# Kernel optimization log

Hardware: AMD Instinct MI355X
Metric: run time of the kernel (lower is better)

## Reference

```python
import jax, jax.numpy as jnp
import numpy as np

N_ENT = 100000
N_REL = 200
D_IN = 128
D_HID = 128
D_OUT = 128
N_BASES = 50
N_EDGES = 800000
N_TRIPLES = 4096
BN_EPS = 1e-5


def setup_inputs() -> dict:
    key = jax.random.key(0)
    ks = jax.random.split(key, 16)
    xavier = lambda k, shape: jax.random.normal(k, shape, jnp.float32) * np.sqrt(2.0 / (shape[-2] + shape[-1]))
    inp = {
        'entity_embeds': xavier(ks[0], (N_ENT, D_IN)),
        'bases': xavier(ks[1], (N_BASES, D_IN)),
        'coefficients': xavier(ks[2], (N_REL, N_BASES)),
        'self_rel_embed': xavier(ks[3], (1, D_IN)),
        'W1': xavier(ks[4], (3, D_IN, D_HID)),
        'relw1': xavier(ks[5], (D_IN, D_HID)),
        'bn1_gamma': jnp.ones((D_HID,), jnp.float32),
        'bn1_beta': jnp.zeros((D_HID,), jnp.float32),
        'W2': xavier(ks[6], (3, D_HID, D_OUT)),
        'relw2': xavier(ks[7], (D_HID, D_OUT)),
        'bn2_gamma': jnp.ones((D_OUT,), jnp.float32),
        'bn2_beta': jnp.zeros((D_OUT,), jnp.float32),
        'ent_ids': jnp.arange(N_ENT, dtype=jnp.int32),
        'edge_index': jax.random.randint(ks[8], (2, N_EDGES), 0, N_ENT, jnp.int32),
        'edge_type': jax.random.randint(ks[9], (N_EDGES,), 0, 2 * N_REL + 1, jnp.int32),
        'y': jax.random.randint(ks[10], (N_EDGES,), 0, 3, jnp.int32),
    }
    heads = jax.random.randint(ks[11], (N_TRIPLES,), 0, N_ENT, jnp.int32)
    rels = jax.random.randint(ks[12], (N_TRIPLES,), 0, 2 * N_REL + 1, jnp.int32)
    tails = jax.random.randint(ks[13], (N_TRIPLES,), 0, N_ENT, jnp.int32)
    inp['triples'] = jnp.stack([heads, rels, tails], axis=1)
    return inp


def _compgcn_layer(x, r, edge_index, edge_type, y, W, relw, gamma, beta):
    src, dst = edge_index[0], edge_index[1]
    # message: gather neighbor & relation embeds, edge-direction-conditioned matmul
    msgs = x[src] - r[edge_type]                      # [E, d_in]
    out = jnp.zeros((msgs.shape[0], W.shape[-1]), msgs.dtype)
    for k in range(3):  # y in {0,1,2}: masked matmul instead of [E,d,d] gather
        mask = (y == k)[:, None]
        out = out + jnp.where(mask, msgs, 0.0) @ W[k]
    # scatter-add aggregation at destination nodes
    agg = jax.ops.segment_sum(out, dst, num_segments=x.shape[0])  # [N, d_out]
    # BatchNorm1d (training-mode batch statistics, biased var)
    mean = jnp.mean(agg, axis=0)
    var = jnp.mean(jnp.square(agg - mean), axis=0)
    bn = (agg - mean) * jax.lax.rsqrt(var + BN_EPS) * gamma + beta
    return jnp.tanh(bn), r @ relw


def reference(entity_embeds, bases, coefficients, self_rel_embed, W1, relw1,
              bn1_gamma, bn1_beta, W2, relw2, bn2_gamma, bn2_beta,
              ent_ids, edge_index, edge_type, y, triples):
    x = entity_embeds[ent_ids]
    r = coefficients @ bases                           # basis-composed relations
    r = jnp.concatenate([r, -r, self_rel_embed], axis=0)  # [2R+1, d]
    x, r = _compgcn_layer(x, r, edge_index, edge_type, y, W1, relw1, bn1_gamma, bn1_beta)
    x, r = _compgcn_layer(x, r, edge_index, edge_type, y, W2, relw2, bn2_gamma, bn2_beta)
    # decode: TransE-style L1 score
    h = x[triples[:, 0]]
    re = r[triples[:, 1]]
    t = x[triples[:, 2]]
    scores = jnp.sum(jnp.abs(h + re - t), axis=1)      # p=1 norm
    return scores
```

## Files before the change

### kernel.cpp

```cpp
#include <hip/hip_runtime.h>
#include <cstdint>

typedef __attribute__((ext_vector_type(8))) short short8;
typedef __attribute__((ext_vector_type(4))) float f32x4;

static __device__ __forceinline__ unsigned short f2bf(float f) {
  unsigned int u = __float_as_uint(f);
  unsigned int r = (u + 0x7FFFu + ((u >> 16) & 1u)) >> 16;
  return (unsigned short)r;
}
static __device__ __forceinline__ unsigned int pack2bf(float a, float b) {
  return (unsigned int)f2bf(a) | ((unsigned int)f2bf(b) << 16);
}
static __device__ __forceinline__ float2 bf2f(unsigned int u) {
  return make_float2(__uint_as_float(u << 16), __uint_as_float(u & 0xFFFF0000u));
}
static __device__ __forceinline__ void acc8(float* a, uint4 h, uint4 r) {
  float2 f, g;
  f = bf2f(h.x); g = bf2f(r.x); a[0] += f.x - g.x; a[1] += f.y - g.y;
  f = bf2f(h.y); g = bf2f(r.y); a[2] += f.x - g.x; a[3] += f.y - g.y;
  f = bf2f(h.z); g = bf2f(r.z); a[4] += f.x - g.x; a[5] += f.y - g.y;
  f = bf2f(h.w); g = bf2f(r.w); a[6] += f.x - g.x; a[7] += f.y - g.y;
}

__global__ __launch_bounds__(256) void k_prep(
    const float* __restrict__ coeff, const float* __restrict__ bases,
    const float* __restrict__ selfr, const float* __restrict__ relw1,
    const float* __restrict__ relw2,
    unsigned int* __restrict__ rfb, unsigned int* __restrict__ r1b,
    float* __restrict__ r2,
    const float* __restrict__ W1, const float* __restrict__ W2,
    unsigned short* __restrict__ WT1, unsigned short* __restrict__ WT2,
    const float* __restrict__ ent, const int* __restrict__ ent_ids,
    unsigned int* __restrict__ entbf,
    int* __restrict__ counts, float* __restrict__ stats,
    int nPairs, int nKeys, int cvtB, int cntB) {
  int b = blockIdx.x, tid = threadIdx.x;
  if (b < 201) {
    __shared__ float row[2][128], r1row[2][128];
    int half = tid >> 7, c = tid & 127;
    int r = 2 * b + half;
    bool ok = (r <= 400);
    if (ok) {
      float v;
      if (r == 400) {
        v = selfr[c];
      } else {
        int rr = (r < 200) ? r : r - 200;
        float s = 0.f;
#pragma unroll 10
        for (int k = 0; k < 50; ++k) s += coeff[rr * 50 + k] * bases[k * 128 + c];
        v = (r < 200) ? s : -s;
      }
      row[half][c] = v;
    }
    __syncthreads();
    if (ok && c < 64) rfb[r * 64 + c] = pack2bf(row[half][2 * c], row[half][2 * c + 1]);
    if (ok) {
      float s = 0.f;
#pragma unroll 8
      for (int k = 0; k < 128; ++k) s += row[half][k] * relw1[k * 128 + c];
      r1row[half][c] = s;
    }
    __syncthreads();
    if (ok && c < 64) r1b[r * 64 + c] = pack2bf(r1row[half][2 * c], r1row[half][2 * c + 1]);
    if (ok) {
      float s = 0.f;
#pragma unroll 8
      for (int k = 0; k < 128; ++k) s += r1row[half][k] * relw2[k * 128 + c];
      r2[r * 128 + c] = s;
    }
  } else if (b < 585) {
    int idx = (b - 201) * 256 + tid;
    const int half = 128 * 384;
    const float* W = (idx < half) ? W1 : W2;
    unsigned short* WT = (idx < half) ? WT1 : WT2;
    int id2 = (idx < half) ? idx : idx - half;
    int n = id2 & 127, k = id2 >> 7;
    int kk = k >> 7, kr = k & 127;
    WT[(size_t)n * 384 + k] = f2bf(W[(size_t)kk * 16384 + kr * 128 + n]);
  } else if (b < 585 + cvtB) {
    int i = (b - 585) * 256 + tid;
    if (i < nPairs) {
      int e = i >> 6;
      int src = ent_ids[e];
      float2 v = *(const float2*)&ent[(size_t)src * 128 + (i & 63) * 2];
      entbf[i] = pack2bf(v.x, v.y);
    }
  } else if (b < 585 + cvtB + cntB) {
    int i = (b - (585 + cvtB)) * 256 + tid;
    if (i < nKeys) counts[i] = 0;
  } else {
    int i = (b - (585 + cvtB + cntB)) * 256 + tid;
    if (i < 16896) stats[i] = 0.f;
  }
}

__global__ __launch_bounds__(256) void k_histR(const int* __restrict__ ei, const int* __restrict__ y,
                                               int* __restrict__ counts, int nE, int rsz) {
  int r = blockIdx.x;
  int e0 = blockIdx.y * 1024;
#pragma unroll
  for (int i = 0; i < 4; ++i) {
    int e = e0 + i * 256 + threadIdx.x;
    if (e < nE) {
      int key = ei[nE + e] * 3 + y[e];
      if (key / rsz == r) atomicAdd(&counts[key], 1);
    }
  }
}

__global__ void k_scan1(const int* __restrict__ counts, int* __restrict__ local,
                        int* __restrict__ blockSums, int n) {
  __shared__ int sdata[1024];
  int tid = threadIdx.x;
  int i = blockIdx.x * 1024 + tid;
  int v = (i < n) ? counts[i] : 0;
  sdata[tid] = v;
  __syncthreads();
  for (int off = 1; off < 1024; off <<= 1) {
    int t = (tid >= off) ? sdata[tid - off] : 0;
    __syncthreads();
    sdata[tid] += t;
    __syncthreads();
  }
  if (i < n) local[i] = sdata[tid] - v;
  if (tid == 1023) blockSums[blockIdx.x] = sdata[1023];
}

__global__ void k_scan2(const int* __restrict__ blockSums, int* __restrict__ carries,
                        int* __restrict__ offsets, int n, int nb) {
  __shared__ int sdata[1024];
  int tid = threadIdx.x;
  int v = (tid < nb) ? blockSums[tid] : 0;
  sdata[tid] = v;
  __syncthreads();
  for (int off = 1; off < 1024; off <<= 1) {
    int t = (tid >= off) ? sdata[tid - off] : 0;
    __syncthreads();
    sdata[tid] += t;
    __syncthreads();
  }
  if (tid < nb) carries[tid] = sdata[tid] - v;
  if (tid == 1023) offsets[n] = sdata[1023];
}

__global__ void k_scan3(const int* __restrict__ local, const int* __restrict__ carries,
                        int* __restrict__ offsets, int* __restrict__ cursor, int n) {
  int i = blockIdx.x * 1024 + threadIdx.x;
  if (i >= n) return;
  int v = local[i] + carries[blockIdx.x];
  offsets[i] = v;
  cursor[i] = v;
}

__global__ __launch_bounds__(256) void k_fillR(const int* __restrict__ ei, const int* __restrict__ et,
                                               const int* __restrict__ y, int* __restrict__ cursor,
                                               unsigned int* __restrict__ bucket, int nE, int rsz) {
  int r = blockIdx.x;
  int e0 = blockIdx.y * 1024;
#pragma unroll
  for (int i = 0; i < 4; ++i) {
    int e = e0 + i * 256 + threadIdx.x;
    if (e < nE) {
      int key = ei[nE + e] * 3 + y[e];
      if (key / rsz == r) {
        int slot = atomicAdd(&cursor[key], 1);
        bucket[slot] = (unsigned int)ei[e] | ((unsigned int)et[e] << 20);
      }
    }
  }
}

__global__ __launch_bounds__(256, 6) void k_fused(
    const unsigned int* __restrict__ xb, const unsigned int* __restrict__ rb,
    const int* __restrict__ offsets, const unsigned int* __restrict__ packed,
    const unsigned short* __restrict__ WT, unsigned short* __restrict__ C,
    float* __restrict__ statsRep, int M) {
  __shared__ unsigned short As[32][392];
  __shared__ float sSum[128], sSq[128];
  const int tid = threadIdx.x;
  const int m0 = blockIdx.x * 32;
  const int wave = tid >> 6, lane = tid & 63;
  const int quad = lane >> 4, l16 = lane & 15;
  const int qid = (wave << 2) | quad;
  if (tid < 128) { sSum[tid] = 0.f; sSq[tid] = 0.f; }

#pragma unroll 1
  for (int i = 0; i < 6; ++i) {
    int kloc = qid * 6 + i;
    int dloc = kloc / 3, cls = kloc - dloc * 3;
    float a0[8] = {}, a1[8] = {};
    int dst = m0 + dloc;
    if (dst < M) {
      int key = dst * 3 + cls;
      int s = offsets[key], e = offsets[key + 1];
      int j = s;
      for (; j + 1 < e; j += 2) {
        unsigned int p0 = packed[j], p1 = packed[j + 1];
        int s0 = p0 & 0xFFFFF, t0 = p0 >> 20;
        int s1 = p1 & 0xFFFFF, t1 = p1 >> 20;
        uint4 h0 = *(const uint4*)&xb[(size_t)s0 * 64 + l16 * 4];
        uint4 r0 = *(const uint4*)&rb[(size_t)t0 * 64 + l16 * 4];
        uint4 h1 = *(const uint4*)&xb[(size_t)s1 * 64 + l16 * 4];
        uint4 r1 = *(const uint4*)&rb[(size_t)t1 * 64 + l16 * 4];
        acc8(a0, h0, r0);
        acc8(a1, h1, r1);
      }
      if (j < e) {
        unsigned int p0 = packed[j];
        int s0 = p0 & 0xFFFFF, t0 = p0 >> 20;
        uint4 h0 = *(const uint4*)&xb[(size_t)s0 * 64 + l16 * 4];
        uint4 r0 = *(const uint4*)&rb[(size_t)t0 * 64 + l16 * 4];
        acc8(a0, h0, r0);
      }
    }
    uint4 o;
    o.x = pack2bf(a0[0] + a1[0], a0[1] + a1[1]);
    o.y = pack2bf(a0[2] + a1[2], a0[3] + a1[3]);
    o.z = pack2bf(a0[4] + a1[4], a0[5] + a1[5]);
    o.w = pack2bf(a0[6] + a1[6], a0[7] + a1[7]);
    *(uint4*)&As[dloc][cls * 128 + l16 * 8] = o;
  }
  __syncthreads();

  const unsigned short* Wp = WT + (size_t)(wave * 32 + l16) * 384 + quad * 8;
  short8 bc0 = *(const short8*)(Wp);
  short8 bc1 = *(const short8*)(Wp + 16 * 384);
  f32x4 acc[2][2] = {};
#pragma unroll 1
  for (int it = 0; it < 12; ++it) {
    short8 bn0, bn1;
    if (it < 11) {
      bn0 = *(const short8*)(Wp + (it + 1) * 32);
      bn1 = *(const short8*)(Wp + 16 * 384 + (it + 1) * 32);
    }
    short8 a[2];
#pragma unroll
    for (int t = 0; t < 2; ++t) a[t] = *(const short8*)&As[t * 16 + l16][it * 32 + quad * 8];
#pragma unroll
    for (int t = 0; t < 2; ++t) {
      acc[t][0] = __builtin_amdgcn_mfma_f32_16x16x32_bf16(a[t], bc0, acc[t][0], 0, 0, 0);
      acc[t][1] = __builtin_amdgcn_mfma_f32_16x16x32_bf16(a[t], bc1, acc[t][1], 0, 0, 0);
    }
    if (it < 11) { bc0 = bn0; bc1 = bn1; }
  }

  float ps[2] = {}, pq[2] = {};
#pragma unroll
  for (int t = 0; t < 2; ++t) {
#pragma unroll
    for (int reg = 0; reg < 4; ++reg) {
      int m = m0 + t * 16 + quad * 4 + reg;
      if (m < M) {
#pragma unroll
        for (int ct = 0; ct < 2; ++ct) {
          float v = acc[t][ct][reg];
          int col = wave * 32 + ct * 16 + l16;
          C[(size_t)m * 128 + col] = f2bf(v);
          ps[ct] += v; pq[ct] += v * v;
        }
      }
    }
  }
#pragma unroll
  for (int ct = 0; ct < 2; ++ct) {
    int col = wave * 32 + ct * 16 + l16;
    atomicAdd(&sSum[col], ps[ct]);
    atomicAdd(&sSq[col], pq[ct]);
  }
  __syncthreads();
  if (tid < 128) {
    float* rep = statsRep + ((blockIdx.x & 31) << 8);
    atomicAdd(&rep[tid], sSum[tid]);
    atomicAdd(&rep[128 + tid], sSq[tid]);
  }
}

__global__ void k_collapse(const float* __restrict__ rep, float* __restrict__ fin) {
  int c = threadIdx.x;
  float s = 0.f;
#pragma unroll
  for (int r = 0; r < 32; ++r) s += rep[r * 256 + c];
  fin[c] = s;
}

__global__ void k_norm(const uint4* __restrict__ Cb4,
                       const float* __restrict__ sums, const float* __restrict__ sumsq,
                       const float* __restrict__ gamma, const float* __restrict__ beta,
                       float invN, uint4* __restrict__ xb4, int nQuad) {
  __shared__ float sc_s[128], bi_s[128];
  if (threadIdx.x < 128) {
    int c = threadIdx.x;
    float mean = sums[c] * invN;
    float var = fmaxf(sumsq[c] * invN - mean * mean, 0.f);
    float sc = rsqrtf(var + 1e-5f) * gamma[c];
    sc_s[c] = sc;
    bi_s[c] = beta[c] - mean * sc;
  }
  __syncthreads();
  int i = blockIdx.x * blockDim.x + threadIdx.x;
  if (i >= nQuad) return;
  uint4 v = Cb4[i];
  int j = (i * 4) & 63;
  uint4 o;
  float2 f;
  f = bf2f(v.x);
  o.x = pack2bf(tanhf(fmaf(f.x, sc_s[2*j],   bi_s[2*j])),   tanhf(fmaf(f.y, sc_s[2*j+1], bi_s[2*j+1])));
  f = bf2f(v.y);
  o.y = pack2bf(tanhf(fmaf(f.x, sc_s[2*j+2], bi_s[2*j+2])), tanhf(fmaf(f.y, sc_s[2*j+3], bi_s[2*j+3])));
  f = bf2f(v.z);
  o.z = pack2bf(tanhf(fmaf(f.x, sc_s[2*j+4], bi_s[2*j+4])), tanhf(fmaf(f.y, sc_s[2*j+5], bi_s[2*j+5])));
  f = bf2f(v.w);
  o.w = pack2bf(tanhf(fmaf(f.x, sc_s[2*j+6], bi_s[2*j+6])), tanhf(fmaf(f.y, sc_s[2*j+7], bi_s[2*j+7])));
  xb4[i] = o;
}

__global__ void k_score(const unsigned int* __restrict__ xb, const float* __restrict__ r,
                        const int* __restrict__ triples, float* __restrict__ out, int nT) {
  int gid = blockIdx.x * blockDim.x + threadIdx.x;
  int t = gid >> 6;
  if (t >= nT) return;
  int lane = gid & 63;
  int h = triples[t * 3], rel = triples[t * 3 + 1], tl = triples[t * 3 + 2];
  float2 a = bf2f(xb[(size_t)h * 64 + lane]);
  float2 b = *(const float2*)&r[(size_t)rel * 128 + lane * 2];
  float2 cc = bf2f(xb[(size_t)tl * 64 + lane]);
  float s = fabsf(a.x + b.x - cc.x) + fabsf(a.y + b.y - cc.y);
#pragma unroll
  for (int off = 32; off > 0; off >>= 1) s += __shfl_down(s, off);
  if (lane == 0) out[t] = s;
}

extern "C" void kernel_launch(void* const* d_in, const int* in_sizes, int n_in,
                              void* d_out, int out_size, void* d_ws, size_t ws_size,
                              hipStream_t stream) {
  const float* ent   = (const float*)d_in[0];
  const float* bases = (const float*)d_in[1];
  const float* coeff = (const float*)d_in[2];
  const float* selfr = (const float*)d_in[3];
  const float* W1    = (const float*)d_in[4];
  const float* relw1 = (const float*)d_in[5];
  const float* g1    = (const float*)d_in[6];
  const float* b1    = (const float*)d_in[7];
  const float* W2    = (const float*)d_in[8];
  const float* relw2 = (const float*)d_in[9];
  const float* g2    = (const float*)d_in[10];
  const float* b2    = (const float*)d_in[11];
  const int* ent_ids = (const int*)d_in[12];
  const int* ei      = (const int*)d_in[13];
  const int* et      = (const int*)d_in[14];
  const int* yk      = (const int*)d_in[15];
  const int* triples = (const int*)d_in[16];

  const int M  = in_sizes[0] / 128;
  const int nE = in_sizes[14];
  const int nT = in_sizes[16] / 3;
  const int nKeys = M * 3;
  const int nScanBlocks = (nKeys + 1023) / 1024;
  const int rsz = (nKeys + 7) / 8;

  float* p = (float*)d_ws;
  float* r2    = p; p += 401 * 128;
  float* statsAll = p; p += 16896;
  float* rep1 = statsAll;
  float* rep2 = statsAll + 32 * 256;
  float* fin1 = statsAll + 64 * 256;
  float* fin2 = fin1 + 256;
  unsigned short* Cb  = (unsigned short*)p;
  unsigned int* entbf = (unsigned int*)(Cb + (size_t)M * 128);
  unsigned int* xb    = entbf + (size_t)M * 64;
  unsigned int* rfb   = xb + (size_t)M * 64;
  unsigned int* r1b   = rfb + 401 * 64;
  unsigned short* WT1 = (unsigned short*)(r1b + 401 * 64);
  unsigned short* WT2 = WT1 + 128 * 384;
  int* counts  = (int*)(WT2 + 128 * 384);
  int* offsets = counts + nKeys;
  int* cursor  = offsets + nKeys + 1;
  int* slocal  = cursor + nKeys;
  int* sblock  = slocal + nKeys;
  int* scarry  = sblock + nScanBlocks;
  unsigned int* bucket = (unsigned int*)(scarry + nScanBlocks);

  float* out = (float*)d_out;

  const int nPairs = M * 64;
  const int nQuad  = M * 16;
  const int cvtB = (nPairs + 255) / 256;
  const int cntB = (nKeys + 255) / 256;
  const int zeroB = 66;
  const int prepBlocks = 585 + cvtB + cntB + zeroB;
  const int fusedBlocks = (M + 31) / 32;
  const int normBlocks = (nQuad + 255) / 256;
  const dim3 rangedGrid(8, (nE + 1023) / 1024);

  k_prep<<<prepBlocks, 256, 0, stream>>>(coeff, bases, selfr, relw1, relw2,
                                         rfb, r1b, r2, W1, W2, WT1, WT2,
                                         ent, ent_ids, entbf, counts, statsAll,
                                         nPairs, nKeys, cvtB, cntB);

  k_histR<<<rangedGrid, 256, 0, stream>>>(ei, yk, counts, nE, rsz);
  k_scan1<<<nScanBlocks, 1024, 0, stream>>>(counts, slocal, sblock, nKeys);
  k_scan2<<<1, 1024, 0, stream>>>(sblock, scarry, offsets, nKeys, nScanBlocks);
  k_scan3<<<nScanBlocks, 1024, 0, stream>>>(slocal, scarry, offsets, cursor, nKeys);
  k_fillR<<<rangedGrid, 256, 0, stream>>>(ei, et, yk, cursor, bucket, nE, rsz);

  k_fused<<<fusedBlocks, 256, 0, stream>>>(entbf, rfb, offsets, bucket, WT1,
                                           Cb, rep1, M);
  k_collapse<<<1, 256, 0, stream>>>(rep1, fin1);
  k_norm<<<normBlocks, 256, 0, stream>>>((const uint4*)Cb, fin1, fin1 + 128, g1, b1,
                                         1.0f / M, (uint4*)xb, nQuad);

  k_fused<<<fusedBlocks, 256, 0, stream>>>(xb, r1b, offsets, bucket, WT2,
                                           Cb, rep2, M);
  k_collapse<<<1, 256, 0, stream>>>(rep2, fin2);
  k_norm<<<normBlocks, 256, 0, stream>>>((const uint4*)Cb, fin2, fin2 + 128, g2, b2,
                                         1.0f / M, (uint4*)xb, nQuad);

  k_score<<<(nT * 64 + 255) / 256, 256, 0, stream>>>(xb, r2, triples, out, nT);
}
```

Baseline: 432.6 us.

## Process edge classes sequentially with a smaller shared tile to raise occupancy

The fused gather+MFMA kernel now loops over the three edge classes. For each class it gathers 32 rows by 128 columns into a shared tile, then runs the four k-steps of the matmul against that class's slice of W. This shrinks shared memory from 32x392 to 32x136 bf16, and launch bounds go from 6 to 8 blocks per CU. The aim is more resident waves to hide gather latency, paid for with two extra barriers per class and less independent gather work per thread between syncs.

After: 450.1 us. 4.1% more time.

```diff
diff --git a/kernel.cpp b/kernel.cpp
--- a/kernel.cpp
+++ b/kernel.cpp
@@ -172,12 +172,12 @@
   }
 }
 
-__global__ __launch_bounds__(256, 6) void k_fused(
+__global__ __launch_bounds__(256, 8) void k_fused(
     const unsigned int* __restrict__ xb, const unsigned int* __restrict__ rb,
     const int* __restrict__ offsets, const unsigned int* __restrict__ packed,
     const unsigned short* __restrict__ WT, unsigned short* __restrict__ C,
     float* __restrict__ statsRep, int M) {
-  __shared__ unsigned short As[32][392];
+  __shared__ unsigned short As[32][136];
   __shared__ float sSum[128], sSq[128];
   const int tid = threadIdx.x;
   const int m0 = blockIdx.x * 32;
@@ -186,64 +186,61 @@
   const int qid = (wave << 2) | quad;
   if (tid < 128) { sSum[tid] = 0.f; sSq[tid] = 0.f; }
 
+  f32x4 acc[2][2] = {};
+  const unsigned short* Wp = WT + (size_t)(wave * 32 + l16) * 384 + quad * 8;
+
 #pragma unroll 1
-  for (int i = 0; i < 6; ++i) {
-    int kloc = qid * 6 + i;
-    int dloc = kloc / 3, cls = kloc - dloc * 3;
-    float a0[8] = {}, a1[8] = {};
-    int dst = m0 + dloc;
-    if (dst < M) {
-      int key = dst * 3 + cls;
-      int s = offsets[key], e = offsets[key + 1];
-      int j = s;
-      for (; j + 1 < e; j += 2) {
-        unsigned int p0 = packed[j], p1 = packed[j + 1];
-        int s0 = p0 & 0xFFFFF, t0 = p0 >> 20;
-        int s1 = p1 & 0xFFFFF, t1 = p1 >> 20;
-        uint4 h0 = *(const uint4*)&xb[(size_t)s0 * 64 + l16 * 4];
-        uint4 r0 = *(const uint4*)&rb[(size_t)t0 * 64 + l16 * 4];
-        uint4 h1 = *(const uint4*)&xb[(size_t)s1 * 64 + l16 * 4];
-        uint4 r1 = *(const uint4*)&rb[(size_t)t1 * 64 + l16 * 4];
-        acc8(a0, h0, r0);
-        acc8(a1, h1, r1);
+  for (int cls = 0; cls < 3; ++cls) {
+#pragma unroll 1
+    for (int i = 0; i < 2; ++i) {
+      int dloc = 2 * qid + i;
+      float a0[8] = {}, a1[8] = {};
+      int dst = m0 + dloc;
+      if (dst < M) {
+        int key = dst * 3 + cls;
+        int s = offsets[key], e = offsets[key + 1];
+        int j = s;
+        for (; j + 1 < e; j += 2) {
+          unsigned int p0 = packed[j], p1 = packed[j + 1];
+          int s0 = p0 & 0xFFFFF, t0 = p0 >> 20;
+          int s1 = p1 & 0xFFFFF, t1 = p1 >> 20;
+          uint4 h0 = *(const uint4*)&xb[(size_t)s0 * 64 + l16 * 4];
+          uint4 r0 = *(const uint4*)&rb[(size_t)t0 * 64 + l16 * 4];
+          uint4 h1 = *(const uint4*)&xb[(size_t)s1 * 64 + l16 * 4];
+          uint4 r1 = *(const uint4*)&rb[(size_t)t1 * 64 + l16 * 4];
+          acc8(a0, h0, r0);
+          acc8(a1, h1, r1);
+        }
+        if (j < e) {
+          unsigned int p0 = packed[j];
+          int s0 = p0 & 0xFFFFF, t0 = p0 >> 20;
+          uint4 h0 = *(const uint4*)&xb[(size_t)s0 * 64 + l16 * 4];
+          uint4 r0 = *(const uint4*)&rb[(size_t)t0 * 64 + l16 * 4];
+          acc8(a0, h0, r0);
+        }
       }
-      if (j < e) {
-        unsigned int p0 = packed[j];
-        int s0 = p0 & 0xFFFFF, t0 = p0 >> 20;
-        uint4 h0 = *(const uint4*)&xb[(size_t)s0 * 64 + l16 * 4];
-        uint4 r0 = *(const uint4*)&rb[(size_t)t0 * 64 + l16 * 4];
-        acc8(a0, h0, r0);
-      }
-    }
-    uint4 o;
-    o.x = pack2bf(a0[0] + a1[0], a0[1] + a1[1]);
-    o.y = pack2bf(a0[2] + a1[2], a0[3] + a1[3]);
-    o.z = pack2bf(a0[4] + a1[4], a0[5] + a1[5]);
-    o.w = pack2bf(a0[6] + a1[6], a0[7] + a1[7]);
-    *(uint4*)&As[dloc][cls * 128 + l16 * 8] = o;
-  }
-  __syncthreads();
-
-  const unsigned short* Wp = WT + (size_t)(wave * 32 + l16) * 384 + quad * 8;
-  short8 bc0 = *(const short8*)(Wp);
-  short8 bc1 = *(const short8*)(Wp + 16 * 384);
-  f32x4 acc[2][2] = {};
-#pragma unroll 1
-  for (int it = 0; it < 12; ++it) {
-    short8 bn0, bn1;
-    if (it < 11) {
-      bn0 = *(const short8*)(Wp + (it + 1) * 32);
-      bn1 = *(const short8*)(Wp + 16 * 384 + (it + 1) * 32);
-    }
-    short8 a[2];
-#pragma unroll
-    for (int t = 0; t < 2; ++t) a[t] = *(const short8*)&As[t * 16 + l16][it * 32 + quad * 8];
-#pragma unroll
-    for (int t = 0; t < 2; ++t) {
-      acc[t][0] = __builtin_amdgcn_mfma_f32_16x16x32_bf16(a[t], bc0, acc[t][0], 0, 0, 0);
-      acc[t][1] = __builtin_amdgcn_mfma_f32_16x16x32_bf16(a[t], bc1, acc[t][1], 0, 0, 0);
-    }
-    if (it < 11) { bc0 = bn0; bc1 = bn1; }
+      uint4 o;
+      o.x = pack2bf(a0[0] + a1[0], a0[1] + a1[1]);
+      o.y = pack2bf(a0[2] + a1[2], a0[3] + a1[3]);
+      o.z = pack2bf(a0[4] + a1[4], a0[5] + a1[5]);
+      o.w = pack2bf(a0[6] + a1[6], a0[7] + a1[7]);
+      *(uint4*)&As[dloc][l16 * 8] = o;
+    }
+    __syncthreads();
+
+    const unsigned short* Wc = Wp + cls * 128;
+#pragma unroll
+    for (int k = 0; k < 4; ++k) {
+      short8 b0 = *(const short8*)(Wc + k * 32);
+      short8 b1 = *(const short8*)(Wc + 16 * 384 + k * 32);
+      short8 a0 = *(const short8*)&As[l16][k * 32 + quad * 8];
+      short8 a1 = *(const short8*)&As[16 + l16][k * 32 + quad * 8];
+      acc[0][0] = __builtin_amdgcn_mfma_f32_16x16x32_bf16(a0, b0, acc[0][0], 0, 0, 0);
+      acc[0][1] = __builtin_amdgcn_mfma_f32_16x16x32_bf16(a0, b1, acc[0][1], 0, 0, 0);
+      acc[1][0] = __builtin_amdgcn_mfma_f32_16x16x32_bf16(a1, b0, acc[1][0], 0, 0, 0);
+      acc[1][1] = __builtin_amdgcn_mfma_f32_16x16x32_bf16(a1, b1, acc[1][1], 0, 0, 0);
+    }
+    __syncthreads();
   }
 
   float ps[2] = {}, pq[2] = {};
```

## Fuse both layers, BN and scoring into one cooperative persistent kernel

Applied to the files above, without the earlier changes.

Replaces the per-layer fused/collapse/norm/score launch sequence with a single cooperative kernel of 1024 blocks, each owning up to four 32-row tiles. The MFMA accumulators stay in registers across a grid-wide sync, so BatchNorm plus tanh are applied directly from registers. This removes the intermediate C buffer round trip and several kernel launches. In exchange it adds grid.sync barriers, higher register pressure from 64 accumulator vectors per thread, and lower occupancy. It keeps a fallback to the old path if the cooperative launch fails.

After: 994.4 us. +129.9%, slower.

```diff
diff --git a/kernel.cpp b/kernel.cpp
--- a/kernel.cpp
+++ b/kernel.cpp
@@ -1,5 +1,8 @@
 #include <hip/hip_runtime.h>
+#include <hip/hip_cooperative_groups.h>
 #include <cstdint>
+
+namespace cg = cooperative_groups;
 
 typedef __attribute__((ext_vector_type(8))) short short8;
 typedef __attribute__((ext_vector_type(4))) float f32x4;
@@ -172,6 +175,200 @@
   }
 }
 
+static __device__ __forceinline__ void gather96(
+    const unsigned int* __restrict__ xb, const unsigned int* __restrict__ rb,
+    const int* __restrict__ offsets, const unsigned int* __restrict__ packed,
+    unsigned short (*As)[392], int m0, int qid, int l16) {
+#pragma unroll 1
+  for (int i = 0; i < 6; ++i) {
+    int kloc = qid * 6 + i;
+    int dloc = kloc / 3, cls = kloc - dloc * 3;
+    float a0[8] = {}, a1[8] = {};
+    int key = (m0 + dloc) * 3 + cls;
+    int s = offsets[key], e = offsets[key + 1];
+    int j = s;
+    for (; j + 1 < e; j += 2) {
+      unsigned int p0 = packed[j], p1 = packed[j + 1];
+      int s0 = p0 & 0xFFFFF, t0 = p0 >> 20;
+      int s1 = p1 & 0xFFFFF, t1 = p1 >> 20;
+      uint4 h0 = *(const uint4*)&xb[(size_t)s0 * 64 + l16 * 4];
+      uint4 r0 = *(const uint4*)&rb[(size_t)t0 * 64 + l16 * 4];
+      uint4 h1 = *(const uint4*)&xb[(size_t)s1 * 64 + l16 * 4];
+      uint4 r1 = *(const uint4*)&rb[(size_t)t1 * 64 + l16 * 4];
+      acc8(a0, h0, r0);
+      acc8(a1, h1, r1);
+    }
+    if (j < e) {
+      unsigned int p0 = packed[j];
+      int s0 = p0 & 0xFFFFF, t0 = p0 >> 20;
+      uint4 h0 = *(const uint4*)&xb[(size_t)s0 * 64 + l16 * 4];
+      uint4 r0 = *(const uint4*)&rb[(size_t)t0 * 64 + l16 * 4];
+      acc8(a0, h0, r0);
+    }
+    uint4 o;
+    o.x = pack2bf(a0[0] + a1[0], a0[1] + a1[1]);
+    o.y = pack2bf(a0[2] + a1[2], a0[3] + a1[3]);
+    o.z = pack2bf(a0[4] + a1[4], a0[5] + a1[5]);
+    o.w = pack2bf(a0[6] + a1[6], a0[7] + a1[7]);
+    *(uint4*)&As[dloc][cls * 128 + l16 * 8] = o;
+  }
+}
+
+struct MegaArgs {
+  const unsigned int* entbf;
+  const unsigned int* rfb;
+  const unsigned int* r1b;
+  const int* offsets;
+  const unsigned int* packed;
+  const unsigned short* WT1;
+  const unsigned short* WT2;
+  float* rep1;
+  float* rep2;
+  const float* g1; const float* b1;
+  const float* g2; const float* b2;
+  unsigned short* xb1;
+  unsigned short* xb2;
+  const float* r2;
+  const int* triples;
+  float* out;
+  int nTiles; int nT; float invN;
+};
+
+static __device__ __forceinline__ void layer_pass(
+    const MegaArgs& A,
+    const unsigned int* __restrict__ xbin, const unsigned int* __restrict__ rbin,
+    const unsigned short* __restrict__ WT, float* __restrict__ rep,
+    const float* __restrict__ gamma, const float* __restrict__ beta,
+    unsigned short* __restrict__ xbout,
+    unsigned short (*As)[392], float* sSum, float* sSq,
+    float* sc_s, float* bi_s, cg::grid_group& grid) {
+  const int tid = threadIdx.x;
+  const int wave = tid >> 6, lane = tid & 63;
+  const int quad = lane >> 4, l16 = lane & 15;
+  const int qid = (wave << 2) | quad;
+  const f32x4 vz = {0.f, 0.f, 0.f, 0.f};
+  f32x4 acc[4][2][2];
+#pragma unroll
+  for (int t = 0; t < 4; ++t)
+#pragma unroll
+    for (int a = 0; a < 2; ++a)
+#pragma unroll
+      for (int b = 0; b < 2; ++b) acc[t][a][b] = vz;
+
+  if (tid < 128) { sSum[tid] = 0.f; sSq[tid] = 0.f; }
+  __syncthreads();
+
+  const unsigned short* Wp = WT + (size_t)(wave * 32 + l16) * 384 + quad * 8;
+
+#pragma unroll
+  for (int t = 0; t < 4; ++t) {
+    int tile = blockIdx.x + t * 1024;
+    bool valid = tile < A.nTiles;
+    if (valid) gather96(xbin, rbin, A.offsets, A.packed, As, tile * 32, qid, l16);
+    __syncthreads();
+    if (valid) {
+      short8 bc0 = *(const short8*)(Wp);
+      short8 bc1 = *(const short8*)(Wp + 16 * 384);
+#pragma unroll 1
+      for (int it = 0; it < 12; ++it) {
+        short8 bn0, bn1;
+        if (it < 11) {
+          bn0 = *(const short8*)(Wp + (it + 1) * 32);
+          bn1 = *(const short8*)(Wp + 16 * 384 + (it + 1) * 32);
+        }
+        short8 a0 = *(const short8*)&As[l16][it * 32 + quad * 8];
+        short8 a1 = *(const short8*)&As[16 + l16][it * 32 + quad * 8];
+        acc[t][0][0] = __builtin_amdgcn_mfma_f32_16x16x32_bf16(a0, bc0, acc[t][0][0], 0, 0, 0);
+        acc[t][0][1] = __builtin_amdgcn_mfma_f32_16x16x32_bf16(a0, bc1, acc[t][0][1], 0, 0, 0);
+        acc[t][1][0] = __builtin_amdgcn_mfma_f32_16x16x32_bf16(a1, bc0, acc[t][1][0], 0, 0, 0);
+        acc[t][1][1] = __builtin_amdgcn_mfma_f32_16x16x32_bf16(a1, bc1, acc[t][1][1], 0, 0, 0);
+        if (it < 11) { bc0 = bn0; bc1 = bn1; }
+      }
+      float ps[2] = {}, pq[2] = {};
+#pragma unroll
+      for (int tr = 0; tr < 2; ++tr)
+#pragma unroll
+        for (int reg = 0; reg < 4; ++reg)
+#pragma unroll
+          for (int ct = 0; ct < 2; ++ct) {
+            float v = acc[t][tr][ct][reg];
+            ps[ct] += v; pq[ct] += v * v;
+          }
+#pragma unroll
+      for (int ct = 0; ct < 2; ++ct) {
+        int col = wave * 32 + ct * 16 + l16;
+        atomicAdd(&sSum[col], ps[ct]);
+        atomicAdd(&sSq[col], pq[ct]);
+      }
+    }
+    __syncthreads();
+  }
+  if (tid < 128) {
+    float* rp = rep + ((blockIdx.x & 31) << 8);
+    atomicAdd(&rp[tid], sSum[tid]);
+    atomicAdd(&rp[128 + tid], sSq[tid]);
+  }
+  grid.sync();
+
+  if (tid < 128) {
+    float s = 0.f, q = 0.f;
+#pragma unroll
+    for (int r = 0; r < 32; ++r) { s += rep[r * 256 + tid]; q += rep[r * 256 + 128 + tid]; }
+    float mean = s * A.invN;
+    float var = fmaxf(q * A.invN - mean * mean, 0.f);
+    float sc = rsqrtf(var + 1e-5f) * gamma[tid];
+    sc_s[tid] = sc;
+    bi_s[tid] = beta[tid] - mean * sc;
+  }
+  __syncthreads();
+
+#pragma unroll
+  for (int t = 0; t < 4; ++t) {
+    int tile = blockIdx.x + t * 1024;
+    if (tile < A.nTiles) {
+      int m0 = tile * 32;
+#pragma unroll
+      for (int tr = 0; tr < 2; ++tr)
+#pragma unroll
+        for (int reg = 0; reg < 4; ++reg) {
+          int m = m0 + tr * 16 + quad * 4 + reg;
+#pragma unroll
+          for (int ct = 0; ct < 2; ++ct) {
+            int col = wave * 32 + ct * 16 + l16;
+            float f = tanhf(fmaf(acc[t][tr][ct][reg], sc_s[col], bi_s[col]));
+            xbout[(size_t)m * 128 + col] = f2bf(f);
+          }
+        }
+    }
+  }
+  grid.sync();
+}
+
+__global__ __launch_bounds__(256, 4) void k_mega(MegaArgs A) {
+  __shared__ unsigned short As[32][392];
+  __shared__ float sSum[128], sSq[128], sc_s[128], bi_s[128];
+  cg::grid_group grid = cg::this_grid();
+
+  layer_pass(A, A.entbf, A.rfb, A.WT1, A.rep1, A.g1, A.b1, A.xb1,
+             As, sSum, sSq, sc_s, bi_s, grid);
+  layer_pass(A, (const unsigned int*)A.xb1, A.r1b, A.WT2, A.rep2, A.g2, A.b2, A.xb2,
+             As, sSum, sSq, sc_s, bi_s, grid);
+
+  int gw = blockIdx.x * 4 + (threadIdx.x >> 6);
+  if (gw < A.nT) {
+    int lane = threadIdx.x & 63;
+    const unsigned int* xbu = (const unsigned int*)A.xb2;
+    int h = A.triples[gw * 3], rel = A.triples[gw * 3 + 1], tl = A.triples[gw * 3 + 2];
+    float2 a = bf2f(xbu[(size_t)h * 64 + lane]);
+    float2 b = *(const float2*)&A.r2[(size_t)rel * 128 + lane * 2];
+    float2 c = bf2f(xbu[(size_t)tl * 64 + lane]);
+    float s = fabsf(a.x + b.x - c.x) + fabsf(a.y + b.y - c.y);
+#pragma unroll
+    for (int off = 32; off > 0; off >>= 1) s += __shfl_down(s, off);
+    if (lane == 0) A.out[gw] = s;
+  }
+}
+
 __global__ __launch_bounds__(256, 6) void k_fused(
     const unsigned int* __restrict__ xb, const unsigned int* __restrict__ rb,
     const int* __restrict__ offsets, const unsigned int* __restrict__ packed,
@@ -185,45 +382,8 @@
   const int quad = lane >> 4, l16 = lane & 15;
   const int qid = (wave << 2) | quad;
   if (tid < 128) { sSum[tid] = 0.f; sSq[tid] = 0.f; }
-
-#pragma unroll 1
-  for (int i = 0; i < 6; ++i) {
-    int kloc = qid * 6 + i;
-    int dloc = kloc / 3, cls = kloc - dloc * 3;
-    float a0[8] = {}, a1[8] = {};
-    int dst = m0 + dloc;
-    if (dst < M) {
-      int key = dst * 3 + cls;
-      int s = offsets[key], e = offsets[key + 1];
-      int j = s;
-      for (; j + 1 < e; j += 2) {
-        unsigned int p0 = packed[j], p1 = packed[j + 1];
-        int s0 = p0 & 0xFFFFF, t0 = p0 >> 20;
-        int s1 = p1 & 0xFFFFF, t1 = p1 >> 20;
-        uint4 h0 = *(const uint4*)&xb[(size_t)s0 * 64 + l16 * 4];
-        uint4 r0 = *(const uint4*)&rb[(size_t)t0 * 64 + l16 * 4];
-        uint4 h1 = *(const uint4*)&xb[(size_t)s1 * 64 + l16 * 4];
-        uint4 r1 = *(const uint4*)&rb[(size_t)t1 * 64 + l16 * 4];
-        acc8(a0, h0, r0);
-        acc8(a1, h1, r1);
-      }
-      if (j < e) {
-        unsigned int p0 = packed[j];
-        int s0 = p0 & 0xFFFFF, t0 = p0 >> 20;
-        uint4 h0 = *(const uint4*)&xb[(size_t)s0 * 64 + l16 * 4];
-        uint4 r0 = *(const uint4*)&rb[(size_t)t0 * 64 + l16 * 4];
-        acc8(a0, h0, r0);
-      }
-    }
-    uint4 o;
-    o.x = pack2bf(a0[0] + a1[0], a0[1] + a1[1]);
-    o.y = pack2bf(a0[2] + a1[2], a0[3] + a1[3]);
-    o.z = pack2bf(a0[4] + a1[4], a0[5] + a1[5]);
-    o.w = pack2bf(a0[6] + a1[6], a0[7] + a1[7]);
-    *(uint4*)&As[dloc][cls * 128 + l16 * 8] = o;
-  }
-  __syncthreads();
-
+  gather96(xb, rb, offsets, packed, As, m0, qid, l16);
+  __syncthreads();
   const unsigned short* Wp = WT + (size_t)(wave * 32 + l16) * 384 + quad * 8;
   short8 bc0 = *(const short8*)(Wp);
   short8 bc1 = *(const short8*)(Wp + 16 * 384);
@@ -235,20 +395,17 @@
       bn0 = *(const short8*)(Wp + (it + 1) * 32);
       bn1 = *(const short8*)(Wp + 16 * 384 + (it + 1) * 32);
     }
-    short8 a[2];
-#pragma unroll
-    for (int t = 0; t < 2; ++t) a[t] = *(const short8*)&As[t * 16 + l16][it * 32 + quad * 8];
-#pragma unroll
-    for (int t = 0; t < 2; ++t) {
-      acc[t][0] = __builtin_amdgcn_mfma_f32_16x16x32_bf16(a[t], bc0, acc[t][0], 0, 0, 0);
-      acc[t][1] = __builtin_amdgcn_mfma_f32_16x16x32_bf16(a[t], bc1, acc[t][1], 0, 0, 0);
-    }
+    short8 a0 = *(const short8*)&As[l16][it * 32 + quad * 8];
+    short8 a1 = *(const short8*)&As[16 + l16][it * 32 + quad * 8];
+    acc[0][0] = __builtin_amdgcn_mfma_f32_16x16x32_bf16(a0, bc0, acc[0][0], 0, 0, 0);
+    acc[0][1] = __builtin_amdgcn_mfma_f32_16x16x32_bf16(a0, bc1, acc[0][1], 0, 0, 0);
+    acc[1][0] = __builtin_amdgcn_mfma_f32_16x16x32_bf16(a1, bc0, acc[1][0], 0, 0, 0);
+    acc[1][1] = __builtin_amdgcn_mfma_f32_16x16x32_bf16(a1, bc1, acc[1][1], 0, 0, 0);
     if (it < 11) { bc0 = bn0; bc1 = bn1; }
   }
-
   float ps[2] = {}, pq[2] = {};
 #pragma unroll
-  for (int t = 0; t < 2; ++t) {
+  for (int t = 0; t < 2; ++t)
 #pragma unroll
     for (int reg = 0; reg < 4; ++reg) {
       int m = m0 + t * 16 + quad * 4 + reg;
@@ -262,7 +419,6 @@
         }
       }
     }
-  }
 #pragma unroll
   for (int ct = 0; ct < 2; ++ct) {
     int col = wave * 32 + ct * 16 + l16;
@@ -368,9 +524,10 @@
   float* fin1 = statsAll + 64 * 256;
   float* fin2 = fin1 + 256;
   unsigned short* Cb  = (unsigned short*)p;
-  unsigned int* entbf = (unsigned int*)(Cb + (size_t)M * 128);
-  unsigned int* xb    = entbf + (size_t)M * 64;
-  unsigned int* rfb   = xb + (size_t)M * 64;
+  unsigned short* xb1 = Cb + (size_t)M * 128;
+  unsigned short* xb2 = xb1 + (size_t)M * 128;
+  unsigned int* entbf = (unsigned int*)(xb2 + (size_t)M * 128);
+  unsigned int* rfb   = entbf + (size_t)M * 64;
   unsigned int* r1b   = rfb + 401 * 64;
   unsigned short* WT1 = (unsigned short*)(r1b + 401 * 64);
   unsigned short* WT2 = WT1 + 128 * 384;
@@ -390,8 +547,7 @@
   const int cntB = (nKeys + 255) / 256;
   const int zeroB = 66;
   const int prepBlocks = 585 + cvtB + cntB + zeroB;
-  const int fusedBlocks = (M + 31) / 32;
-  const int normBlocks = (nQuad + 255) / 256;
+  const int nTiles = (M + 31) / 32;
   const dim3 rangedGrid(8, (nE + 1023) / 1024);
 
   k_prep<<<prepBlocks, 256, 0, stream>>>(coeff, bases, selfr, relw1, relw2,
@@ -405,17 +561,31 @@
   k_scan3<<<nScanBlocks, 1024, 0, stream>>>(slocal, scarry, offsets, cursor, nKeys);
   k_fillR<<<rangedGrid, 256, 0, stream>>>(ei, et, yk, cursor, bucket, nE, rsz);
 
-  k_fused<<<fusedBlocks, 256, 0, stream>>>(entbf, rfb, offsets, bucket, WT1,
-                                           Cb, rep1, M);
-  k_collapse<<<1, 256, 0, stream>>>(rep1, fin1);
-  k_norm<<<normBlocks, 256, 0, stream>>>((const uint4*)Cb, fin1, fin1 + 128, g1, b1,
-                                         1.0f / M, (uint4*)xb, nQuad);
-
-  k_fused<<<fusedBlocks, 256, 0, stream>>>(xb, r1b, offsets, bucket, WT2,
-                                           Cb, rep2, M);
-  k_collapse<<<1, 256, 0, stream>>>(rep2, fin2);
-  k_norm<<<normBlocks, 256, 0, stream>>>((const uint4*)Cb, fin2, fin2 + 128, g2, b2,
-                                         1.0f / M, (uint4*)xb, nQuad);
-
-  k_score<<<(nT * 64 + 255) / 256, 256, 0, stream>>>(xb, r2, triples, out, nT);
-}
+  MegaArgs margs;
+  margs.entbf = entbf; margs.rfb = rfb; margs.r1b = r1b;
+  margs.offsets = offsets; margs.packed = bucket;
+  margs.WT1 = WT1; margs.WT2 = WT2;
+  margs.rep1 = rep1; margs.rep2 = rep2;
+  margs.g1 = g1; margs.b1 = b1; margs.g2 = g2; margs.b2 = b2;
+  margs.xb1 = xb1; margs.xb2 = xb2;
+  margs.r2 = r2; margs.triples = triples; margs.out = out;
+  margs.nTiles = nTiles; margs.nT = nT; margs.invN = 1.0f / M;
+  void* kargs[] = {(void*)&margs};
+  hipError_t merr = hipLaunchCooperativeKernel((const void*)k_mega, dim3(1024), dim3(256),
+                                               kargs, 0, stream);
+  if (merr != hipSuccess) {
+    const int fusedBlocks = nTiles;
+    const int normBlocks = (nQuad + 255) / 256;
+    k_fused<<<fusedBlocks, 256, 0, stream>>>(entbf, rfb, offsets, bucket, WT1, Cb, rep1, M);
+    k_collapse<<<1, 256, 0, stream>>>(rep1, fin1);
+    k_norm<<<normBlocks, 256, 0, stream>>>((const uint4*)Cb, fin1, fin1 + 128, g1, b1,
+                                           1.0f / M, (uint4*)xb1, nQuad);
+    k_fused<<<fusedBlocks, 256, 0, stream>>>((const unsigned int*)xb1, r1b, offsets, bucket,
+                                             WT2, Cb, rep2, M);
+    k_collapse<<<1, 256, 0, stream>>>(rep2, fin2);
+    k_norm<<<normBlocks, 256, 0, stream>>>((const uint4*)Cb, fin2, fin2 + 128, g2, b2,
+                                           1.0f / M, (uint4*)xb2, nQuad);
+    k_score<<<(nT * 64 + 255) / 256, 256, 0, stream>>>((const unsigned int*)xb2, r2,
+                                                       triples, out, nT);
+  }
+}
```

## Stream all six segments per quad with software-pipelined gathers; fold collapse into norm

Applied to the files above, without the earlier changes.

Each 16-lane quad now handles two consecutive destination nodes (six class segments) as one contiguous edge range. It prefetches the next pair of edge gathers while accumulating the current pair, and flushes to LDS at segment boundaries. The aim is to hide gather latency across segments that are short (about 2-3 edges each) and to drop the per-segment loop overhead and tails. The separate k_collapse launch is removed, and each k_norm block now reduces the 32 replica partials itself, which adds redundant reads but saves two launches. The flush lambda and the boundary clamping add control-flow divergence and register pressure.

Result: faster. 399.5 us (-7.6%).

```diff
diff --git a/kernel.cpp b/kernel.cpp
--- a/kernel.cpp
+++ b/kernel.cpp
@@ -186,41 +186,77 @@
   const int qid = (wave << 2) | quad;
   if (tid < 128) { sSum[tid] = 0.f; sSq[tid] = 0.f; }
 
-#pragma unroll 1
-  for (int i = 0; i < 6; ++i) {
-    int kloc = qid * 6 + i;
-    int dloc = kloc / 3, cls = kloc - dloc * 3;
-    float a0[8] = {}, a1[8] = {};
-    int dst = m0 + dloc;
-    if (dst < M) {
-      int key = dst * 3 + cls;
-      int s = offsets[key], e = offsets[key + 1];
-      int j = s;
-      for (; j + 1 < e; j += 2) {
-        unsigned int p0 = packed[j], p1 = packed[j + 1];
-        int s0 = p0 & 0xFFFFF, t0 = p0 >> 20;
-        int s1 = p1 & 0xFFFFF, t1 = p1 >> 20;
-        uint4 h0 = *(const uint4*)&xb[(size_t)s0 * 64 + l16 * 4];
-        uint4 r0 = *(const uint4*)&rb[(size_t)t0 * 64 + l16 * 4];
-        uint4 h1 = *(const uint4*)&xb[(size_t)s1 * 64 + l16 * 4];
-        uint4 r1 = *(const uint4*)&rb[(size_t)t1 * 64 + l16 * 4];
-        acc8(a0, h0, r0);
-        acc8(a1, h1, r1);
+  {
+    const int dst0 = m0 + 2 * qid;
+    int b0, b1, b2, b3, b4, b5, b6;
+    if (dst0 + 1 < M) {
+      const int base = dst0 * 3;
+      b0 = offsets[base];     b1 = offsets[base + 1];
+      b2 = offsets[base + 2]; b3 = offsets[base + 3];
+      b4 = offsets[base + 4]; b5 = offsets[base + 5];
+      b6 = offsets[base + 6];
+    } else if (dst0 < M) {
+      const int base = dst0 * 3;
+      b0 = offsets[base];     b1 = offsets[base + 1];
+      b2 = offsets[base + 2]; b3 = offsets[base + 3];
+      b4 = b3; b5 = b3; b6 = b3;
+    } else {
+      b0 = b1 = b2 = b3 = b4 = b5 = b6 = 0;
+    }
+    float ac[8] = {};
+    int seg = 0;
+    int nextB = b1;
+    int j = b0;
+    const int hi = b6;
+    unsigned short* lds0 = &As[2 * qid][0];
+
+    auto flushSeg = [&]() {
+      int rowOff = (seg >= 3) ? 392 : 0;
+      int cls = seg - ((seg >= 3) ? 3 : 0);
+      uint4 ov;
+      ov.x = pack2bf(ac[0], ac[1]);
+      ov.y = pack2bf(ac[2], ac[3]);
+      ov.z = pack2bf(ac[4], ac[5]);
+      ov.w = pack2bf(ac[6], ac[7]);
+      *(uint4*)(lds0 + rowOff + cls * 128 + l16 * 8) = ov;
+#pragma unroll
+      for (int z = 0; z < 8; ++z) ac[z] = 0.f;
+      ++seg;
+      nextB = (seg == 1) ? b2 : (seg == 2) ? b3 : (seg == 3) ? b4
+            : (seg == 4) ? b5 : b6;
+    };
+
+    if (j < hi) {
+      int jc1 = (j + 1 < hi) ? j + 1 : j;
+      unsigned int q0 = packed[j], q1 = packed[jc1];
+      int s0 = q0 & 0xFFFFF, t0 = q0 >> 20;
+      int s1 = q1 & 0xFFFFF, t1 = q1 >> 20;
+      uint4 h0 = *(const uint4*)&xb[(size_t)s0 * 64 + l16 * 4];
+      uint4 r0 = *(const uint4*)&rb[(size_t)t0 * 64 + l16 * 4];
+      uint4 h1 = *(const uint4*)&xb[(size_t)s1 * 64 + l16 * 4];
+      uint4 r1 = *(const uint4*)&rb[(size_t)t1 * 64 + l16 * 4];
+      while (j < hi) {
+        int jp2 = (j + 2 < hi) ? j + 2 : hi - 1;
+        int jp3 = (j + 3 < hi) ? j + 3 : hi - 1;
+        unsigned int q2 = packed[jp2], q3 = packed[jp3];
+        int s2 = q2 & 0xFFFFF, t2 = q2 >> 20;
+        int s3 = q3 & 0xFFFFF, t3 = q3 >> 20;
+        uint4 th0 = *(const uint4*)&xb[(size_t)s2 * 64 + l16 * 4];
+        uint4 tr0 = *(const uint4*)&rb[(size_t)t2 * 64 + l16 * 4];
+        uint4 th1 = *(const uint4*)&xb[(size_t)s3 * 64 + l16 * 4];
+        uint4 tr1 = *(const uint4*)&rb[(size_t)t3 * 64 + l16 * 4];
+        while (j == nextB) flushSeg();
+        acc8(ac, h0, r0);
+        ++j;
+        if (j < hi) {
+          while (j == nextB) flushSeg();
+          acc8(ac, h1, r1);
+          ++j;
+        }
+        h0 = th0; r0 = tr0; h1 = th1; r1 = tr1;
       }
-      if (j < e) {
-        unsigned int p0 = packed[j];
-        int s0 = p0 & 0xFFFFF, t0 = p0 >> 20;
-        uint4 h0 = *(const uint4*)&xb[(size_t)s0 * 64 + l16 * 4];
-        uint4 r0 = *(const uint4*)&rb[(size_t)t0 * 64 + l16 * 4];
-        acc8(a0, h0, r0);
-      }
-    }
-    uint4 o;
-    o.x = pack2bf(a0[0] + a1[0], a0[1] + a1[1]);
-    o.y = pack2bf(a0[2] + a1[2], a0[3] + a1[3]);
-    o.z = pack2bf(a0[4] + a1[4], a0[5] + a1[5]);
-    o.w = pack2bf(a0[6] + a1[6], a0[7] + a1[7]);
-    *(uint4*)&As[dloc][cls * 128 + l16 * 8] = o;
+    }
+    while (seg < 6) flushSeg();
   }
   __syncthreads();
 
@@ -235,20 +271,18 @@
       bn0 = *(const short8*)(Wp + (it + 1) * 32);
       bn1 = *(const short8*)(Wp + 16 * 384 + (it + 1) * 32);
     }
-    short8 a[2];
-#pragma unroll
-    for (int t = 0; t < 2; ++t) a[t] = *(const short8*)&As[t * 16 + l16][it * 32 + quad * 8];
-#pragma unroll
-    for (int t = 0; t < 2; ++t) {
-      acc[t][0] = __builtin_amdgcn_mfma_f32_16x16x32_bf16(a[t], bc0, acc[t][0], 0, 0, 0);
-      acc[t][1] = __builtin_amdgcn_mfma_f32_16x16x32_bf16(a[t], bc1, acc[t][1], 0, 0, 0);
-    }
+    short8 a0 = *(const short8*)&As[l16][it * 32 + quad * 8];
+    short8 a1 = *(const short8*)&As[16 + l16][it * 32 + quad * 8];
+    acc[0][0] = __builtin_amdgcn_mfma_f32_16x16x32_bf16(a0, bc0, acc[0][0], 0, 0, 0);
+    acc[0][1] = __builtin_amdgcn_mfma_f32_16x16x32_bf16(a0, bc1, acc[0][1], 0, 0, 0);
+    acc[1][0] = __builtin_amdgcn_mfma_f32_16x16x32_bf16(a1, bc0, acc[1][0], 0, 0, 0);
+    acc[1][1] = __builtin_amdgcn_mfma_f32_16x16x32_bf16(a1, bc1, acc[1][1], 0, 0, 0);
     if (it < 11) { bc0 = bn0; bc1 = bn1; }
   }
 
   float ps[2] = {}, pq[2] = {};
 #pragma unroll
-  for (int t = 0; t < 2; ++t) {
+  for (int t = 0; t < 2; ++t)
 #pragma unroll
     for (int reg = 0; reg < 4; ++reg) {
       int m = m0 + t * 16 + quad * 4 + reg;
@@ -262,7 +296,6 @@
         }
       }
     }
-  }
 #pragma unroll
   for (int ct = 0; ct < 2; ++ct) {
     int col = wave * 32 + ct * 16 + l16;
@@ -277,23 +310,20 @@
   }
 }
 
-__global__ void k_collapse(const float* __restrict__ rep, float* __restrict__ fin) {
-  int c = threadIdx.x;
-  float s = 0.f;
-#pragma unroll
-  for (int r = 0; r < 32; ++r) s += rep[r * 256 + c];
-  fin[c] = s;
-}
-
-__global__ void k_norm(const uint4* __restrict__ Cb4,
-                       const float* __restrict__ sums, const float* __restrict__ sumsq,
+__global__ void k_norm(const uint4* __restrict__ Cb4, const float* __restrict__ rep,
                        const float* __restrict__ gamma, const float* __restrict__ beta,
                        float invN, uint4* __restrict__ xb4, int nQuad) {
   __shared__ float sc_s[128], bi_s[128];
   if (threadIdx.x < 128) {
     int c = threadIdx.x;
-    float mean = sums[c] * invN;
-    float var = fmaxf(sumsq[c] * invN - mean * mean, 0.f);
+    float s = 0.f, q = 0.f;
+#pragma unroll
+    for (int r = 0; r < 32; ++r) {
+      s += rep[r * 256 + c];
+      q += rep[r * 256 + 128 + c];
+    }
+    float mean = s * invN;
+    float var = fmaxf(q * invN - mean * mean, 0.f);
     float sc = rsqrtf(var + 1e-5f) * gamma[c];
     sc_s[c] = sc;
     bi_s[c] = beta[c] - mean * sc;
@@ -365,8 +395,6 @@
   float* statsAll = p; p += 16896;
   float* rep1 = statsAll;
   float* rep2 = statsAll + 32 * 256;
-  float* fin1 = statsAll + 64 * 256;
-  float* fin2 = fin1 + 256;
   unsigned short* Cb  = (unsigned short*)p;
   unsigned int* entbf = (unsigned int*)(Cb + (size_t)M * 128);
   unsigned int* xb    = entbf + (size_t)M * 64;
@@ -407,14 +435,12 @@
 
   k_fused<<<fusedBlocks, 256, 0, stream>>>(entbf, rfb, offsets, bucket, WT1,
                                            Cb, rep1, M);
-  k_collapse<<<1, 256, 0, stream>>>(rep1, fin1);
-  k_norm<<<normBlocks, 256, 0, stream>>>((const uint4*)Cb, fin1, fin1 + 128, g1, b1,
+  k_norm<<<normBlocks, 256, 0, stream>>>((const uint4*)Cb, rep1, g1, b1,
                                          1.0f / M, (uint4*)xb, nQuad);
 
   k_fused<<<fusedBlocks, 256, 0, stream>>>(xb, r1b, offsets, bucket, WT2,
                                            Cb, rep2, M);
-  k_collapse<<<1, 256, 0, stream>>>(rep2, fin2);
-  k_norm<<<normBlocks, 256, 0, stream>>>((const uint4*)Cb, fin2, fin2 + 128, g2, b2,
+  k_norm<<<normBlocks, 256, 0, stream>>>((const uint4*)Cb, rep2, g2, b2,
                                          1.0f / M, (uint4*)xb, nQuad);
 
   k_score<<<(nT * 64 + 255) / 256, 256, 0, stream>>>(xb, r2, triples, out, nT);
```
